# Optimization experiments

Hardware: AMD Instinct MI355X
Metric: run time of the kernel (lower is better)

The kernel has to match this reference:

```python
import jax, jax.numpy as jnp
import numpy as np

HEADS = (4, 2, 1)
OUTS = (32, 16, 2)
NEG_SLOPE = 0.2


def gat_conv(x, src, dst, W, att_s, att_d, b, heads, out_dim, n_nodes, concat):
    # x: [N, Fin] -> h: [N, H, Fout]
    h = (x @ W).reshape(n_nodes, heads, out_dim)
    # per-node attention terms, gathered to edges: [E, H]
    a_src = jnp.sum(h * att_s, axis=-1)
    a_dst = jnp.sum(h * att_d, axis=-1)
    logits = jax.nn.leaky_relu(a_src[src] + a_dst[dst], NEG_SLOPE)
    # segment softmax over incoming edges of each destination node
    lmax = jax.ops.segment_max(logits, dst, num_segments=n_nodes)[dst]
    e = jnp.exp(logits - lmax)
    denom = jax.ops.segment_sum(e, dst, num_segments=n_nodes)[dst]
    alpha = e / denom  # [E, H]
    # weighted message aggregation
    msg = h[src] * alpha[:, :, None]  # [E, H, Fout]
    agg = jax.ops.segment_sum(msg, dst, num_segments=n_nodes)  # [N, H, Fout]
    if concat:
        agg = agg.reshape(n_nodes, heads * out_dim)
    else:
        agg = agg.mean(axis=1)
    return agg + b


def _glorot(key, shape):
    fan = shape[0] + shape[-1] if len(shape) == 2 else shape[-1] * 2
    s = jnp.sqrt(6.0 / fan)
    return jax.random.uniform(key, shape, jnp.float32, -s, s)


def setup_inputs() -> dict:
    key = jax.random.key(0)
    N, E, FIN = 100000, 1600000, 128
    ks = jax.random.split(key, 16)
    x = jax.random.normal(ks[0], (N, FIN), jnp.float32)
    edge_index = jax.random.randint(ks[1], (2, E), 0, N, jnp.int64)
    ins = (FIN, HEADS[0] * OUTS[0], HEADS[1] * OUTS[1])
    d = {"x": x, "edge_index": edge_index}
    for i in range(3):
        H, O = HEADS[i], OUTS[i]
        d[f"W{i+1}"] = _glorot(ks[2 + 4 * i], (ins[i], H * O))
        d[f"att_s{i+1}"] = _glorot(ks[3 + 4 * i], (H, O))
        d[f"att_d{i+1}"] = _glorot(ks[4 + 4 * i], (H, O))
        bdim = H * O if i < 2 else O
        d[f"b{i+1}"] = jnp.zeros((bdim,), jnp.float32)
    return d


def reference(x, edge_index, W1, att_s1, att_d1, b1, W2, att_s2, att_d2, b2, W3, att_s3, att_d3, b3):
    N = x.shape[0]
    loops = jnp.arange(N, dtype=edge_index.dtype)
    src = jnp.concatenate([edge_index[0], loops])
    dst = jnp.concatenate([edge_index[1], loops])
    h = gat_conv(x, src, dst, W1, att_s1, att_d1, b1, HEADS[0], OUTS[0], N, True)
    h = jax.nn.elu(h)
    h = gat_conv(h, src, dst, W2, att_s2, att_d2, b2, HEADS[1], OUTS[1], N, True)
    h = jax.nn.elu(h)
    h = gat_conv(h, src, dst, W3, att_s3, att_d3, b3, HEADS[2], OUTS[2], N, False)
    return jax.nn.log_softmax(h, axis=1)
```

## Files before the change

kernel.cpp:

```cpp
#include <hip/hip_runtime.h>
#include <math.h>

static __device__ __forceinline__ float lrelu(float x){ return fmaxf(x, 0.2f*x); }
static __device__ __forceinline__ float eluf(float x){ return x > 0.f ? x : __expf(x)-1.f; }
static __device__ __forceinline__ float fexp2(float x){ return __builtin_amdgcn_exp2f(x); }
static __device__ __forceinline__ unsigned short f2bf(float f){
  unsigned int u = __float_as_uint(f);
  unsigned int r = (u + 0x7FFFu + ((u>>16)&1u)) >> 16;
  return (unsigned short)r;
}
static __device__ __forceinline__ float bflo(unsigned int u){ return __uint_as_float(u<<16); }
static __device__ __forceinline__ float bfhi(unsigned int u){ return __uint_as_float(u & 0xFFFF0000u); }

#define LOG2E 1.44269504f
#define CLAMP2 115.41f
#define ECAP 4096

typedef __attribute__((ext_vector_type(8))) short short8;
typedef __attribute__((ext_vector_type(4))) float f32x4;

static __device__ __forceinline__ uint4 ld16(const uint4* base, unsigned eoff){
  return *(const uint4*)((const char*)base + (size_t)(eoff*16u));
}
static __device__ __forceinline__ float ldf(const float* base, unsigned eoff){
  return *(const float*)((const char*)base + (size_t)(eoff*4u));
}

#define DETECT_IS64(ei_, s_is64_) \
  if (threadIdx.x < 64){ \
    int w_ = ((const int*)(ei_))[2*threadIdx.x + 1]; \
    unsigned long long b_ = __ballot(w_ != 0); \
    if (threadIdx.x == 0) s_is64_ = (b_ == 0ull); \
  } \
  __syncthreads();

__global__ void k_wprep(const float* __restrict__ W1, const float* __restrict__ W2,
                        unsigned short* __restrict__ wf1, unsigned short* __restrict__ wf2,
                        int* __restrict__ gcnt, int NB){
  int e = blockIdx.x*256 + threadIdx.x;
  if (e < NB) gcnt[e] = 0;
  if (e < 2048){
    int lane = e&63, ct = (e>>6)&7, ks = e>>9;
    int q = lane>>4, n = lane&15;
    union { unsigned short us[8]; uint4 u; } pk;
    #pragma unroll
    for (int j=0;j<8;j++)
      pk.us[j] = f2bf(W1[(ks*32 + q*8 + j)*128 + ct*16 + n]);
    *(uint4*)&wf1[(size_t)e*8] = pk.u;
  } else if (e < 2048+512){
    int e2 = e - 2048;
    int lane = e2&63, ct = (e2>>6)&1, ks = e2>>7;
    int q = lane>>4, n = lane&15;
    union { unsigned short us[8]; uint4 u; } pk;
    #pragma unroll
    for (int j=0;j<8;j++)
      pk.us[j] = f2bf(W2[(ks*32 + q*8 + j)*32 + ct*16 + n]);
    *(uint4*)&wf2[(size_t)e2*8] = pk.u;
  }
}

#define BS_ITEMS 16
__global__ __launch_bounds__(256) void k_scat_gemm1(
    const void* __restrict__ ei, int* __restrict__ gcnt,
    unsigned int* __restrict__ ebuf, int E, int NB, int GS,
    const float* __restrict__ x, const unsigned short* __restrict__ wf,
    const float* __restrict__ atts, const float* __restrict__ attd,
    unsigned short* __restrict__ hb, float* __restrict__ as_, float* __restrict__ ad_,
    int N){
  __shared__ __align__(16) unsigned char smem[50176];
  __shared__ int s_is64;
  int t = threadIdx.x;
  if ((int)blockIdx.x < GS){
    int* lcnt  = (int*)smem;
    int* lbase = lcnt + NB;
    for (int i=t; i<NB; i+=256) lcnt[i]=0;
    DETECT_IS64(ei, s_is64)
    bool is64 = s_is64 != 0;
    int base = blockIdx.x*(256*BS_ITEMS);
    unsigned int ent[BS_ITEMS]; int bk[BS_ITEMS];
    #pragma unroll
    for (int i=0;i<BS_ITEMS;i++){
      int e = base + i*256 + t;
      if (e < E){
        int s, d;
        if (is64){ const long long* p=(const long long*)ei; s=(int)p[e]; d=(int)p[(size_t)E+e]; }
        else     { const int* p=(const int*)ei;            s=p[e];      d=p[(size_t)E+e]; }
        int b = d>>7;
        bk[i] = b;
        ent[i] = (unsigned int)s | ((unsigned int)(d & 127) << 25);
        atomicAdd(&lcnt[b], 1);
      } else bk[i] = -1;
    }
    __syncthreads();
    for (int i=t; i<NB; i+=256){
      int c = lcnt[i];
      lbase[i] = c ? atomicAdd(&gcnt[i], c) : 0;
    }
    __syncthreads();
    for (int i=t; i<NB; i+=256) lcnt[i]=0;
    __syncthreads();
    #pragma unroll
    for (int i=0;i<BS_ITEMS;i++){
      if (bk[i] >= 0){
        int pos = lbase[bk[i]] + atomicAdd(&lcnt[bk[i]], 1);
        if (pos < ECAP)
          ebuf[(size_t)bk[i]*ECAP + pos] = ent[i];
      }
    }
  } else {
    unsigned short* xs  = (unsigned short*)smem;
    unsigned short* wsm = (unsigned short*)(smem + 64*136*2);
    int r0 = ((int)blockIdx.x - GS)*64;
    {
      const uint4* src = (const uint4*)wf;
      uint4* dst = (uint4*)wsm;
      #pragma unroll
      for (int i=0;i<8;i++) dst[t + i*256] = src[t + i*256];
    }
    {
      #pragma unroll
      for (int i=0;i<4;i++){
        int idx = t + i*256;
        int row = idx>>4, k8 = (idx&15)*8;
        int gr = r0 + row;
        float4 v0 = make_float4(0.f,0.f,0.f,0.f), v1 = v0;
        if (gr < N){
          v0 = *(const float4*)&x[(size_t)gr*128 + k8];
          v1 = *(const float4*)&x[(size_t)gr*128 + k8 + 4];
        }
        union { unsigned short us[8]; uint4 u; } pk;
        pk.us[0]=f2bf(v0.x); pk.us[1]=f2bf(v0.y); pk.us[2]=f2bf(v0.z); pk.us[3]=f2bf(v0.w);
        pk.us[4]=f2bf(v1.x); pk.us[5]=f2bf(v1.y); pk.us[6]=f2bf(v1.z); pk.us[7]=f2bf(v1.w);
        *(uint4*)&xs[row*136 + k8] = pk.u;
      }
    }
    __syncthreads();
    int w = t>>6, lane = t&63, lm = lane&15, q = lane>>4;
    int rt0 = (w&1)*2;
    int ct0 = (w>>1)*4;
    f32x4 acc[2][4];
    #pragma unroll
    for (int a=0;a<2;a++)
      #pragma unroll
      for (int c=0;c<4;c++) acc[a][c] = (f32x4){0.f,0.f,0.f,0.f};
    #pragma unroll
    for (int ks=0;ks<4;ks++){
      short8 a0 = *(const short8*)&xs[( rt0   *16 + lm)*136 + ks*32 + q*8];
      short8 a1 = *(const short8*)&xs[((rt0+1)*16 + lm)*136 + ks*32 + q*8];
      #pragma unroll
      for (int c=0;c<4;c++){
        short8 b = *(const short8*)&wsm[((ks*8 + ct0 + c)*64 + lane)*8];
        acc[0][c] = __builtin_amdgcn_mfma_f32_16x16x32_bf16(a0, b, acc[0][c], 0,0,0);
        acc[1][c] = __builtin_amdgcn_mfma_f32_16x16x32_bf16(a1, b, acc[1][c], 0,0,0);
      }
    }
    __syncthreads();
    #pragma unroll
    for (int rl=0;rl<2;rl++)
      #pragma unroll
      for (int c=0;c<4;c++)
        #pragma unroll
        for (int r=0;r<4;r++)
          xs[((rt0+rl)*16 + q*4 + r)*136 + (ct0+c)*16 + lm] = f2bf(acc[rl][c][r]);
    __syncthreads();
    {
      #pragma unroll
      for (int i=0;i<4;i++){
        int idx = t + i*256;
        int row = idx>>4, c8 = (idx&15)*8;
        int gr = r0 + row;
        if (gr < N)
          *(uint4*)&hb[(size_t)gr*128 + c8] = *(const uint4*)&xs[row*136 + c8];
      }
    }
    {
      int row = t>>2, h = t&3;
      int gr = r0 + row;
      if (gr < N){
        const unsigned short* hr = &xs[row*136 + h*32];
        const float* sa = atts + h*32;
        const float* da = attd + h*32;
        float ss = 0.f, dd = 0.f;
        #pragma unroll
        for (int o=0;o<32;o+=8){
          uint4 v = *(const uint4*)&hr[o];
          float hv[8] = { bflo(v.x),bfhi(v.x),bflo(v.y),bfhi(v.y),
                          bflo(v.z),bfhi(v.z),bflo(v.w),bfhi(v.w) };
          #pragma unroll
          for (int m=0;m<8;m++){ ss += hv[m]*sa[o+m]; dd += hv[m]*da[o+m]; }
        }
        as_[gr*4+h] = ss*LOG2E; ad_[gr*4+h] = dd*LOG2E;
      }
    }
  }
}

__global__ __launch_bounds__(256) void k_bcsr(const unsigned int* __restrict__ ebuf,
    const int* __restrict__ gcnt,
    int* __restrict__ rp, int* __restrict__ re, int* __restrict__ csr, int N, int NB){
  __shared__ unsigned int lde[ECAP];
  __shared__ int lcnt[128];
  __shared__ int lexc[128];
  __shared__ int lcur[128];
  __shared__ int sc[256];
  int b = blockIdx.x, t = threadIdx.x;
  int d0 = b<<7;
  int R = N - d0; if (R > 128) R = 128;
  if (t < 128){ lcnt[t]=0; lcur[t]=0; }
  __syncthreads();
  size_t base = (size_t)b*ECAP;
  int cnt = gcnt[b]; if (cnt > ECAP) cnt = ECAP;
  for (int i=t; i<cnt; i+=256){
    unsigned int e = ebuf[base+i];
    lde[i] = e;
    atomicAdd(&lcnt[e>>25], 1);
  }
  __syncthreads();
  int v = (t<128)? lcnt[t] : 0;
  sc[t]=v; __syncthreads();
  for (int off=1; off<128; off<<=1){
    int add = (t>=off)? sc[t-off] : 0;
    __syncthreads();
    sc[t]+=add;
    __syncthreads();
  }
  if (t<128) lexc[t] = sc[t]-v;
  __syncthreads();
  if (t < R){
    int s = (int)base + lexc[t];
    rp[d0+t] = s;
    re[d0+t] = s + lcnt[t];
  }
  for (int i=t; i<cnt; i+=256){
    unsigned int e = lde[i];
    int dl = e>>25;
    int pos = lexc[dl] + atomicAdd(&lcur[dl], 1);
    csr[base + pos] = (int)(e & 0x1FFFFFFu);
  }
}

__global__ __launch_bounds__(256) void k_mgemm2(const unsigned short* __restrict__ xb,
    const unsigned short* __restrict__ wf,
    const float* __restrict__ atts, const float* __restrict__ attd,
    unsigned short* __restrict__ hb2, float* __restrict__ as_, float* __restrict__ ad_,
    int N){
  __shared__ unsigned short xs[128*136];
  __shared__ unsigned short wsm[512*8];
  int t = threadIdx.x;
  int r0 = blockIdx.x*128;
  {
    #pragma unroll
    for (int i=0;i<2;i++)
      ((uint4*)wsm)[t + i*256] = ((const uint4*)wf)[t + i*256];
  }
  {
    #pragma unroll
    for (int i=0;i<8;i++){
      int idx = t + i*256;
      int row = idx>>4, c8 = (idx&15)*8;
      int gr = r0 + row;
      uint4 v = make_uint4(0u,0u,0u,0u);
      if (gr < N) v = *(const uint4*)&xb[(size_t)gr*128 + c8];
      *(uint4*)&xs[row*136 + c8] = v;
    }
  }
  __syncthreads();
  int w = t>>6, lane = t&63, lm = lane&15, q = lane>>4;
  int rt0 = 2*w;
  f32x4 acc[2][2];
  #pragma unroll
  for (int a=0;a<2;a++){ acc[a][0] = (f32x4){0.f,0.f,0.f,0.f}; acc[a][1] = acc[a][0]; }
  #pragma unroll
  for (int ks=0;ks<4;ks++){
    short8 a0 = *(const short8*)&xs[( rt0   *16 + lm)*136 + ks*32 + q*8];
    short8 a1 = *(const short8*)&xs[((rt0+1)*16 + lm)*136 + ks*32 + q*8];
    #pragma unroll
    for (int c=0;c<2;c++){
      short8 b = *(const short8*)&wsm[((ks*2 + c)*64 + lane)*8];
      acc[0][c] = __builtin_amdgcn_mfma_f32_16x16x32_bf16(a0, b, acc[0][c], 0,0,0);
      acc[1][c] = __builtin_amdgcn_mfma_f32_16x16x32_bf16(a1, b, acc[1][c], 0,0,0);
    }
  }
  __syncthreads();
  #pragma unroll
  for (int rl=0;rl<2;rl++)
    #pragma unroll
    for (int c=0;c<2;c++)
      #pragma unroll
      for (int r=0;r<4;r++)
        xs[((rt0+rl)*16 + q*4 + r)*136 + c*16 + lm] = f2bf(acc[rl][c][r]);
  __syncthreads();
  {
    #pragma unroll
    for (int i=0;i<2;i++){
      int idx = t + i*256;
      int row = idx>>2, c8 = (idx&3)*8;
      int gr = r0 + row;
      if (gr < N)
        *(uint4*)&hb2[(size_t)gr*32 + c8] = *(const uint4*)&xs[row*136 + c8];
    }
  }
  {
    int row = t>>1, h = t&1;
    int gr = r0 + row;
    if (gr < N){
      const unsigned short* hr = &xs[row*136 + h*16];
      const float* sa = atts + h*16;
      const float* da = attd + h*16;
      float ss = 0.f, dd = 0.f;
      #pragma unroll
      for (int o=0;o<16;o+=8){
        uint4 v = *(const uint4*)&hr[o];
        float hv[8] = { bflo(v.x),bfhi(v.x),bflo(v.y),bfhi(v.y),
                        bflo(v.z),bfhi(v.z),bflo(v.w),bfhi(v.w) };
        #pragma unroll
        for (int m=0;m<8;m++){ ss += hv[m]*sa[o+m]; dd += hv[m]*da[o+m]; }
      }
      as_[gr*2+h] = ss*LOG2E; ad_[gr*2+h] = dd*LOG2E;
    }
  }
}

#define ACC8(v_, w_) { \
  a[0]+=w_*bflo(v_.x); a[1]+=w_*bfhi(v_.x); a[2]+=w_*bflo(v_.y); a[3]+=w_*bfhi(v_.y); \
  a[4]+=w_*bflo(v_.z); a[5]+=w_*bfhi(v_.z); a[6]+=w_*bflo(v_.w); a[7]+=w_*bfhi(v_.w); }

__global__ __launch_bounds__(256) void k_agg1(const int* __restrict__ rp, const int* __restrict__ re,
    const int* __restrict__ csr,
    const float* __restrict__ as_, const float* __restrict__ ad_,
    const uint4* __restrict__ hb4, const float* __restrict__ bias,
    unsigned short* __restrict__ outb, int N){
  int n = blockIdx.x*16 + (threadIdx.x>>4);
  if (n >= N) return;
  int li = threadIdx.x & 15, ghead = li>>2;
  int start = rp[n], end = re[n];
  float adh = ldf(ad_, (unsigned)n*4u+ghead);
  float a[8];
  #pragma unroll
  for (int k=0;k<8;k++) a[k]=0.f;
  float wse = fexp2(fminf(lrelu(ldf(as_, (unsigned)n*4u+ghead) + adh), CLAMP2));
  float l = wse;
  { uint4 v = ld16(hb4, (unsigned)n*16u + li); ACC8(v, wse) }
  int i = start;
  for (; i + 1 < end; i += 2){
    int s0 = csr[i];
    int s1 = csr[i+1];
    float w0 = fexp2(fminf(lrelu(ldf(as_, (unsigned)s0*4u+ghead) + adh), CLAMP2));
    float w1 = fexp2(fminf(lrelu(ldf(as_, (unsigned)s1*4u+ghead) + adh), CLAMP2));
    uint4 v0 = ld16(hb4, (unsigned)s0*16u + li);
    uint4 v1 = ld16(hb4, (unsigned)s1*16u + li);
    l += w0 + w1;
    ACC8(v0, w0)
    ACC8(v1, w1)
  }
  if (i < end){
    int s = csr[i];
    float w = fexp2(fminf(lrelu(ldf(as_, (unsigned)s*4u+ghead) + adh), CLAMP2));
    uint4 v = ld16(hb4, (unsigned)s*16u + li);
    l += w;
    ACC8(v, w)
  }
  float invh = 1.f/l;
  float4 b0 = *(const float4*)&bias[li*8];
  float4 b1 = *(const float4*)&bias[li*8+4];
  union { unsigned short us[8]; uint4 v; } pk;
  pk.us[0]=f2bf(eluf(a[0]*invh+b0.x)); pk.us[1]=f2bf(eluf(a[1]*invh+b0.y));
  pk.us[2]=f2bf(eluf(a[2]*invh+b0.z)); pk.us[3]=f2bf(eluf(a[3]*invh+b0.w));
  pk.us[4]=f2bf(eluf(a[4]*invh+b1.x)); pk.us[5]=f2bf(eluf(a[5]*invh+b1.y));
  pk.us[6]=f2bf(eluf(a[6]*invh+b1.z)); pk.us[7]=f2bf(eluf(a[7]*invh+b1.w));
  *(uint4*)&outb[(size_t)n*128 + li*8] = pk.v;
}

__global__ __launch_bounds__(256) void k_agg2(const int* __restrict__ rp, const int* __restrict__ re,
    const int* __restrict__ csr,
    const float* __restrict__ as_, const float* __restrict__ ad_,
    const uint4* __restrict__ hb4, const float* __restrict__ bias,
    const float* __restrict__ W3, const float* __restrict__ atts3,
    const float* __restrict__ attd3,
    float4* __restrict__ pk4, int N){
  int n = blockIdx.x*64 + (threadIdx.x>>2);
  if (n >= N) return;
  int li = threadIdx.x & 3, ghead = li>>1;
  int start = rp[n], end = re[n];
  float adh = ldf(ad_, (unsigned)n*2u+ghead);
  float a[8];
  #pragma unroll
  for (int k=0;k<8;k++) a[k]=0.f;
  float wse = fexp2(fminf(lrelu(ldf(as_, (unsigned)n*2u+ghead) + adh), CLAMP2));
  float l = wse;
  { uint4 v = ld16(hb4, (unsigned)n*4u + li); ACC8(v, wse) }
  int i = start;
  for (; i + 1 < end; i += 2){
    int s0 = csr[i];
    int s1 = csr[i+1];
    float w0 = fexp2(fminf(lrelu(ldf(as_, (unsigned)s0*2u+ghead) + adh), CLAMP2));
    float w1 = fexp2(fminf(lrelu(ldf(as_, (unsigned)s1*2u+ghead) + adh), CLAMP2));
    uint4 v0 = ld16(hb4, (unsigned)s0*4u + li);
    uint4 v1 = ld16(hb4, (unsigned)s1*4u + li);
    l += w0 + w1;
    ACC8(v0, w0)
    ACC8(v1, w1)
  }
  if (i < end){
    int s = csr[i];
    float w = fexp2(fminf(lrelu(ldf(as_, (unsigned)s*2u+ghead) + adh), CLAMP2));
    uint4 v = ld16(hb4, (unsigned)s*4u + li);
    l += w;
    ACC8(v, w)
  }
  float invh = 1.f/l;
  float r0_ = eluf(a[0]*invh + bias[li*8+0]);
  float r1_ = eluf(a[1]*invh + bias[li*8+1]);
  float r2_ = eluf(a[2]*invh + bias[li*8+2]);
  float r3_ = eluf(a[3]*invh + bias[li*8+3]);
  float r4_ = eluf(a[4]*invh + bias[li*8+4]);
  float r5_ = eluf(a[5]*invh + bias[li*8+5]);
  float r6_ = eluf(a[6]*invh + bias[li*8+6]);
  float r7_ = eluf(a[7]*invh + bias[li*8+7]);
  const float* wr = &W3[li*16];
  float p0 = r0_*wr[0] + r1_*wr[2] + r2_*wr[4]  + r3_*wr[6]
           + r4_*wr[8] + r5_*wr[10]+ r6_*wr[12] + r7_*wr[14];
  float p1 = r0_*wr[1] + r1_*wr[3] + r2_*wr[5]  + r3_*wr[7]
           + r4_*wr[9] + r5_*wr[11]+ r6_*wr[13] + r7_*wr[15];
  p0 += __shfl_xor(p0,1); p0 += __shfl_xor(p0,2);
  p1 += __shfl_xor(p1,1); p1 += __shfl_xor(p1,2);
  if (li == 0){
    float4 pk;
    pk.x = p0; pk.y = p1;
    pk.z = (p0*atts3[0] + p1*atts3[1])*LOG2E;
    pk.w = (p0*attd3[0] + p1*attd3[1])*LOG2E;
    pk4[n] = pk;
  }
}

__global__ __launch_bounds__(256) void k_agg3(const int* __restrict__ rp, const int* __restrict__ re,
    const int* __restrict__ csr,
    const float4* __restrict__ pk4, const float* __restrict__ bias,
    float* __restrict__ out, int N){
  int n = blockIdx.x*16 + (threadIdx.x>>4);
  if (n >= N) return;
  int li = threadIdx.x & 15;
  int start = rp[n], end = re[n];
  float4 self = pk4[n];
  float adh = self.w;
  float l = 0.f;
  float2 acc = make_float2(0.f, 0.f);
  for (int i=start+li; i<end; i+=16){
    int s = csr[i];
    float4 ps = pk4[s];
    float w = fexp2(fminf(lrelu(ps.z + adh), CLAMP2));
    l += w;
    acc.x += w*ps.x; acc.y += w*ps.y;
  }
  if (li == 0){
    float w = fexp2(fminf(lrelu(self.z + adh), CLAMP2));
    l += w;
    acc.x += w*self.x; acc.y += w*self.y;
  }
  #pragma unroll
  for (int msk=1; msk<16; msk<<=1){
    l += __shfl_xor(l, msk);
    acc.x += __shfl_xor(acc.x, msk);
    acc.y += __shfl_xor(acc.y, msk);
  }
  if (li == 0){
    float inv = 1.f/l;
    float g0 = acc.x*inv + bias[0];
    float g1 = acc.y*inv + bias[1];
    float mm = fmaxf(g0, g1);
    float lse = mm + logf(__expf(g0-mm) + __expf(g1-mm));
    *(float2*)&out[2*n] = make_float2(g0-lse, g1-lse);
  }
}

extern "C" void kernel_launch(void* const* d_in, const int* in_sizes, int n_in,
                              void* d_out, int out_size, void* d_ws, size_t ws_size,
                              hipStream_t stream) {
  const float* x   = (const float*)d_in[0];
  const void*  ei  = d_in[1];
  const float* W1  = (const float*)d_in[2];
  const float* as1 = (const float*)d_in[3];
  const float* ad1 = (const float*)d_in[4];
  const float* b1  = (const float*)d_in[5];
  const float* W2  = (const float*)d_in[6];
  const float* as2 = (const float*)d_in[7];
  const float* ad2 = (const float*)d_in[8];
  const float* b2  = (const float*)d_in[9];
  const float* W3  = (const float*)d_in[10];
  const float* as3 = (const float*)d_in[11];
  const float* ad3 = (const float*)d_in[12];
  const float* b3  = (const float*)d_in[13];

  int N = in_sizes[0] / 128;
  int E = in_sizes[1] / 2;
  int NB = (N + 127) >> 7;

  char* w = (char*)d_ws;
  size_t off = 0;
  auto alloc = [&](size_t bytes)->void*{
    void* p = w + off; off += (bytes + 255) & ~(size_t)255; return p;
  };
  int*   gcnt    = (int*)alloc((size_t)NB*4);
  int*   rp      = (int*)alloc((size_t)N*4);
  int*   re      = (int*)alloc((size_t)N*4);
  unsigned int* ebuf = (unsigned int*)alloc((size_t)NB*ECAP*4);
  int*   csr     = (int*)alloc((size_t)NB*ECAP*4);
  float* as_buf  = (float*)alloc((size_t)N*4*4);
  float* ad_buf  = (float*)alloc((size_t)N*4*4);
  unsigned short* wf1 = (unsigned short*)alloc(2048*8*2);
  unsigned short* wf2 = (unsigned short*)alloc(512*8*2);
  unsigned short* hb  = (unsigned short*)alloc((size_t)N*128*2);
  unsigned short* xb  = (unsigned short*)alloc((size_t)N*128*2);
  unsigned short* hb2 = (unsigned short*)alloc((size_t)N*32*2);
  float4* pk4    = (float4*)alloc((size_t)N*16);
  if (off > ws_size) return;

  k_wprep<<<10, 256, 0, stream>>>(W1, W2, wf1, wf2, gcnt, NB);

  int GS = (E + 256*BS_ITEMS - 1) / (256*BS_ITEMS);
  int G1 = (N + 63)/64;
  k_scat_gemm1<<<GS + G1, 256, 0, stream>>>(ei, gcnt, ebuf, E, NB, GS,
                                            x, wf1, as1, ad1, hb, as_buf, ad_buf, N);
  k_bcsr<<<NB, 256, 0, stream>>>(ebuf, gcnt, rp, re, csr, N, NB);

  k_agg1<<<(N + 15)/16, 256, 0, stream>>>(rp, re, csr, as_buf, ad_buf, (const uint4*)hb, b1, xb, N);

  k_mgemm2<<<(N + 127)/128, 256, 0, stream>>>(xb, wf2, as2, ad2, hb2, as_buf, ad_buf, N);
  k_agg2<<<(N + 63)/64, 256, 0, stream>>>(rp, re, csr, as_buf, ad_buf, (const uint4*)hb2, b2,
                                          W3, as3, ad3, pk4, N);

  k_agg3<<<(N + 15)/16, 256, 0, stream>>>(rp, re, csr, pk4, b3, (float*)d_out, N);
}
```

Measured before the change: 291.0 us.

## Reuse first-pass atomic offsets in bucketing and split agg1 launch in two

```diff
diff --git a/kernel.cpp b/kernel.cpp
--- a/kernel.cpp
+++ b/kernel.cpp
@@ -77,7 +77,7 @@
     DETECT_IS64(ei, s_is64)
     bool is64 = s_is64 != 0;
     int base = blockIdx.x*(256*BS_ITEMS);
-    unsigned int ent[BS_ITEMS]; int bk[BS_ITEMS];
+    unsigned int ent[BS_ITEMS]; int bk[BS_ITEMS]; int lofs[BS_ITEMS];
     #pragma unroll
     for (int i=0;i<BS_ITEMS;i++){
       int e = base + i*256 + t;
@@ -88,7 +88,7 @@
         int b = d>>7;
         bk[i] = b;
         ent[i] = (unsigned int)s | ((unsigned int)(d & 127) << 25);
-        atomicAdd(&lcnt[b], 1);
+        lofs[i] = atomicAdd(&lcnt[b], 1);
       } else bk[i] = -1;
     }
     __syncthreads();
@@ -97,12 +97,10 @@
       lbase[i] = c ? atomicAdd(&gcnt[i], c) : 0;
     }
     __syncthreads();
-    for (int i=t; i<NB; i+=256) lcnt[i]=0;
-    __syncthreads();
     #pragma unroll
     for (int i=0;i<BS_ITEMS;i++){
       if (bk[i] >= 0){
-        int pos = lbase[bk[i]] + atomicAdd(&lcnt[bk[i]], 1);
+        int pos = lbase[bk[i]] + lofs[i];
         if (pos < ECAP)
           ebuf[(size_t)bk[i]*ECAP + pos] = ent[i];
       }
@@ -199,21 +197,21 @@
     const int* __restrict__ gcnt,
     int* __restrict__ rp, int* __restrict__ re, int* __restrict__ csr, int N, int NB){
   __shared__ unsigned int lde[ECAP];
+  __shared__ unsigned short lofp[ECAP];
   __shared__ int lcnt[128];
   __shared__ int lexc[128];
-  __shared__ int lcur[128];
   __shared__ int sc[256];
   int b = blockIdx.x, t = threadIdx.x;
   int d0 = b<<7;
   int R = N - d0; if (R > 128) R = 128;
-  if (t < 128){ lcnt[t]=0; lcur[t]=0; }
+  if (t < 128) lcnt[t]=0;
   __syncthreads();
   size_t base = (size_t)b*ECAP;
   int cnt = gcnt[b]; if (cnt > ECAP) cnt = ECAP;
   for (int i=t; i<cnt; i+=256){
     unsigned int e = ebuf[base+i];
     lde[i] = e;
-    atomicAdd(&lcnt[e>>25], 1);
+    lofp[i] = (unsigned short)atomicAdd(&lcnt[e>>25], 1);
   }
   __syncthreads();
   int v = (t<128)? lcnt[t] : 0;
@@ -233,9 +231,7 @@
   }
   for (int i=t; i<cnt; i+=256){
     unsigned int e = lde[i];
-    int dl = e>>25;
-    int pos = lexc[dl] + atomicAdd(&lcur[dl], 1);
-    csr[base + pos] = (int)(e & 0x1FFFFFFu);
+    csr[base + lexc[e>>25] + lofp[i]] = (int)(e & 0x1FFFFFFu);
   }
 }
 
@@ -329,9 +325,9 @@
     const int* __restrict__ csr,
     const float* __restrict__ as_, const float* __restrict__ ad_,
     const uint4* __restrict__ hb4, const float* __restrict__ bias,
-    unsigned short* __restrict__ outb, int N){
-  int n = blockIdx.x*16 + (threadIdx.x>>4);
-  if (n >= N) return;
+    unsigned short* __restrict__ outb, int n0, int nlim){
+  int n = n0 + blockIdx.x*16 + (threadIdx.x>>4);
+  if (n >= nlim) return;
   int li = threadIdx.x & 15, ghead = li>>2;
   int start = rp[n], end = re[n];
   float adh = ldf(ad_, (unsigned)n*4u+ghead);
@@ -523,7 +519,13 @@
                                             x, wf1, as1, ad1, hb, as_buf, ad_buf, N);
   k_bcsr<<<NB, 256, 0, stream>>>(ebuf, gcnt, rp, re, csr, N, NB);
 
-  k_agg1<<<(N + 15)/16, 256, 0, stream>>>(rp, re, csr, as_buf, ad_buf, (const uint4*)hb, b1, xb, N);
+  int Nh = ((N >> 1) + 15) & ~15;
+  if (Nh > N) Nh = N;
+  k_agg1<<<(Nh + 15)/16, 256, 0, stream>>>(rp, re, csr, as_buf, ad_buf,
+                                           (const uint4*)hb, b1, xb, 0, Nh);
+  if (N > Nh)
+    k_agg1<<<(N - Nh + 15)/16, 256, 0, stream>>>(rp, re, csr, as_buf, ad_buf,
+                                                 (const uint4*)hb, b1, xb, Nh, N);
 
   k_mgemm2<<<(N + 127)/128, 256, 0, stream>>>(xb, wf2, as2, ad2, hb2, as_buf, ad_buf, N);
   k_agg2<<<(N + 63)/64, 256, 0, stream>>>(rp, re, csr, as_buf, ad_buf, (const uint4*)hb2, b2,
```

Measured after the change: 296.8 us. Within noise of the previous version (+2.0%).
